# Optimization experiments

Hardware: AMD Instinct MI355X
Metric: run time of the kernel (lower is better)

## Reference

```python
import jax, jax.numpy as jnp
import numpy as np

M, K, N, E = 8192, 1024, 1024, 8  # total tokens, in-dim, out-dim, experts/segments


def setup_inputs() -> dict:
    key = jax.random.key(0)
    k1, k2, k3 = jax.random.split(key, 3)
    a = jax.random.normal(k1, (M, K), dtype=jnp.float32)
    b = jax.random.normal(k2, (E, N, K), dtype=jnp.float32) * 0.02  # column-major per-expert weights
    c = jnp.zeros((M, N), dtype=jnp.float32)
    inner = jnp.sort(jax.random.randint(k3, (E - 1,), 0, M, dtype=jnp.int32))
    seg_indptr = jnp.concatenate([
        jnp.zeros((1,), jnp.int32), inner, jnp.full((1,), M, jnp.int32)
    ])  # [E+1], monotone, covers [0, M)
    weight_indices = jnp.arange(E, dtype=jnp.int32)
    return {
        "a": a, "b": b, "c": c,
        "batch_size": E, "weight_column_major": 1,
        "seg_indptr": seg_indptr, "weight_indices": weight_indices,
    }


def reference(a, b, c, batch_size, weight_column_major, seg_indptr, weight_indices):
    # Grouped GEMM: for each contiguous segment s of rows [seg_indptr[s], seg_indptr[s+1]),
    # c[rows] = a[rows] @ b[weight_indices[s]].T  (b is [E, N, K], column-major weights).
    assert weight_column_major
    rows = jnp.arange(a.shape[0])[:, None]  # [M, 1]
    out = c
    for s in range(batch_size):  # fixed small loop over experts/segments
        b_e = jnp.take(b, weight_indices[s], axis=0)  # [N, K]
        seg_out = a @ b_e.T                            # [M, N]
        mask = (rows >= seg_indptr[s]) & (rows < seg_indptr[s + 1])
        out = jnp.where(mask, seg_out, out)
    return out
```

## Files before the change

kernel.cpp:

```cpp
#include <hip/hip_runtime.h>
#include <hip/hip_bf16.h>
#include <stdint.h>

#define MDIM 8192
#define KDIM 1024
#define NDIM 1024
#define NEXP 8
#define BM 256
#define BN 256
#define BK 64
#define LDSS 40

typedef __attribute__((ext_vector_type(8))) short bf16x8;
typedef __attribute__((ext_vector_type(4))) float floatx4;
typedef __attribute__((ext_vector_type(8))) unsigned short ushort8;

static __device__ __forceinline__ unsigned short f2b(float f) {
    unsigned int u = __float_as_uint(f);
    return (unsigned short)((u + 0x7fffu + ((u >> 16) & 1u)) >> 16);
}

__global__ __launch_bounds__(256)
void cvt_bf16(const float* __restrict__ a, const float* __restrict__ b,
              unsigned short* __restrict__ wa, unsigned short* __restrict__ wb)
{
    const long t  = (long)blockIdx.x * 256 + threadIdx.x;
    const long NA = (long)MDIM * KDIM / 8;
    const float* src; unsigned short* dst; long v;
    if (t < NA) { src = a; dst = wa; v = t; }
    else        { src = b; dst = wb; v = t - NA; }
    const float4 lo = ((const float4*)src)[2 * v];
    const float4 hi = ((const float4*)src)[2 * v + 1];
    ushort8 o;
    o[0] = f2b(lo.x); o[1] = f2b(lo.y); o[2] = f2b(lo.z); o[3] = f2b(lo.w);
    o[4] = f2b(hi.x); o[5] = f2b(hi.y); o[6] = f2b(hi.z); o[7] = f2b(hi.w);
    ((ushort8*)dst)[v] = o;
}

#define GLDS(gp, lp) __builtin_amdgcn_global_load_lds(                        \
    (const __attribute__((address_space(1))) unsigned int*)(gp),              \
    (__attribute__((address_space(3))) unsigned int*)(lp), 16, 0, 0)

#define BAR asm volatile("s_barrier" ::: "memory")


__global__ __launch_bounds__(512, 2)
void grouped_gemm_v8(const unsigned short* __restrict__ A,
                     const unsigned short* __restrict__ B,
                     const int* __restrict__ seg_indptr,
                     const int* __restrict__ widx,
                     float* __restrict__ c)
{
    alignas(16) __shared__ unsigned short As0[BM * BK], As1[BM * BK];
    alignas(16) __shared__ unsigned short Bs0[BN * BK], Bs1[BN * BK];

    const int orig = (int)blockIdx.x;
    const int xcd = orig & 7, lin = orig >> 3;
    const int bid = (xcd < 4 ? xcd * 20 : 80 + (xcd - 4) * 19) + lin;

    const int NTN = NDIM / BN;
    int rem = bid;
    int s = -1, m0 = 0, seg_end = 0, n0 = 0;
    for (int i = 0; i < NEXP; ++i) {
        int ps = seg_indptr[i], pe = seg_indptr[i + 1];
        int nt = ((pe - ps + BM - 1) / BM) * NTN;
        if (rem < nt) { s = i; m0 = ps + (rem / NTN) * BM; n0 = (rem % NTN) * BN; seg_end = pe; break; }
        rem -= nt;
    }
    if (s < 0) return;

    const unsigned short* __restrict__ be = B + (size_t)widx[s] * (size_t)(NDIM * KDIM);

    const int tid  = (int)threadIdx.x;
    const int wave = tid >> 6;
    const int lane = tid & 63;

    const int srow = tid >> 3;
    const int gch  = ((tid & 7) ^ (srow & 7)) * 8;
    const unsigned short* ap[4];
    const unsigned short* bp[4];
#pragma unroll
    for (int j = 0; j < 4; ++j) {
        int ra = m0 + j * 64 + srow; if (ra >= MDIM) ra = MDIM - 1;
        ap[j] = A  + (size_t)ra * KDIM + gch;
        bp[j] = be + (size_t)(n0 + j * 64 + srow) * KDIM + gch;
    }
    const int ldso = wave * 512;

    const int wm = (wave >> 2) * 128;
    const int wn = (wave & 3) * 64;
    const int fr   = lane & 15;
    const int quad = lane >> 4;
    const int fro0 = ((0 * 4 + quad) ^ (fr & 7)) * 8;
    const int fro1 = ((1 * 4 + quad) ^ (fr & 7)) * 8;

    floatx4 acc[8][4] = {};
    bf16x8 b0[4], b1[4];

#define STAGE_A(DST, h, koff) do {                                            \
        GLDS(ap[2 * (h) + 0] + (koff), &DST[(2 * (h) + 0) * 4096 + ldso]);    \
        GLDS(ap[2 * (h) + 1] + (koff), &DST[(2 * (h) + 1) * 4096 + ldso]);    \
    } while (0)
#define STAGE_B(DST, h, koff) do {                                            \
        GLDS(bp[2 * (h) + 0] + (koff), &DST[(2 * (h) + 0) * 4096 + ldso]);    \
        GLDS(bp[2 * (h) + 1] + (koff), &DST[(2 * (h) + 1) * 4096 + ldso]);    \
    } while (0)

#define PHASE(AS, BS, Q, RB, STG, WV)                                         \
    do {                                                                      \
        bf16x8 af0  = *reinterpret_cast<const bf16x8*>(                       \
            &AS[(wm + (2 * (Q) + 0) * 16 + fr) * BK + fro0]);                 \
        bf16x8 af1  = *reinterpret_cast<const bf16x8*>(                       \
            &AS[(wm + (2 * (Q) + 1) * 16 + fr) * BK + fro0]);                 \
        bf16x8 af0b = *reinterpret_cast<const bf16x8*>(                       \
            &AS[(wm + (2 * (Q) + 0) * 16 + fr) * BK + fro1]);                 \
        bf16x8 af1b = *reinterpret_cast<const bf16x8*>(                       \
            &AS[(wm + (2 * (Q) + 1) * 16 + fr) * BK + fro1]);                 \
        if (RB) {                                                             \
            _Pragma("unroll")                                                 \
            for (int ni = 0; ni < 4; ++ni) {                                  \
                b0[ni] = *reinterpret_cast<const bf16x8*>(                    \
                    &BS[(wn + ni * 16 + fr) * BK + fro0]);                    \
                b1[ni] = *reinterpret_cast<const bf16x8*>(                    \
                    &BS[(wn + ni * 16 + fr) * BK + fro1]);                    \
            }                                                                 \
        }                                                                     \
        STG;                                                                  \
        if (RB) asm volatile("s_waitcnt lgkmcnt(8)" ::: "memory");            \
        BAR;                                                                  \
        asm volatile("s_waitcnt lgkmcnt(0)" ::: "memory");                    \
        __builtin_amdgcn_s_setprio(1);                                        \
        _Pragma("unroll")                                                     \
        for (int ni = 0; ni < 4; ++ni) {                                      \
            acc[2 * (Q) + 0][ni] = __builtin_amdgcn_mfma_f32_16x16x32_bf16(   \
                af0,  b0[ni], acc[2 * (Q) + 0][ni], 0, 0, 0);                 \
            acc[2 * (Q) + 1][ni] = __builtin_amdgcn_mfma_f32_16x16x32_bf16(   \
                af1,  b0[ni], acc[2 * (Q) + 1][ni], 0, 0, 0);                 \
            acc[2 * (Q) + 0][ni] = __builtin_amdgcn_mfma_f32_16x16x32_bf16(   \
                af0b, b1[ni], acc[2 * (Q) + 0][ni], 0, 0, 0);                 \
            acc[2 * (Q) + 1][ni] = __builtin_amdgcn_mfma_f32_16x16x32_bf16(   \
                af1b, b1[ni], acc[2 * (Q) + 1][ni], 0, 0, 0);                 \
        }                                                                     \
        __builtin_amdgcn_s_setprio(0);                                        \
        WV;                                                                   \
        BAR;                                                                  \
    } while (0)

#define VM4 asm volatile("s_waitcnt vmcnt(4)" ::: "memory")

    STAGE_A(As0, 0, 0); STAGE_A(As0, 1, 0);
    STAGE_B(Bs0, 0, 0); STAGE_B(Bs0, 1, 0);
    STAGE_B(Bs1, 0, BK); STAGE_B(Bs1, 1, BK);
    asm volatile("s_waitcnt vmcnt(4)" ::: "memory");
    BAR;

#pragma unroll 1
    for (int ii = 0; ii < 8; ++ii) {
        const int t   = 2 * ii;
        const int kA1 = (t + 1) * BK;
        const int kN2 = ((t + 2) & 15) * BK;
        const int kN3 = ((t + 3) & 15) * BK;
        PHASE(As0, Bs0, 0, true,  STAGE_A(As1, 0, kA1), (void)0);
        PHASE(As0, Bs0, 1, false, STAGE_A(As1, 1, kA1), (void)0);
        PHASE(As0, Bs0, 2, false, STAGE_B(Bs0, 0, kN2), (void)0);
        PHASE(As0, Bs0, 3, false, STAGE_B(Bs0, 1, kN2), VM4);
        PHASE(As1, Bs1, 0, true,  STAGE_A(As0, 0, kN2), (void)0);
        PHASE(As1, Bs1, 1, false, STAGE_A(As0, 1, kN2), (void)0);
        PHASE(As1, Bs1, 2, false, STAGE_B(Bs1, 0, kN3), (void)0);
        PHASE(As1, Bs1, 3, false, STAGE_B(Bs1, 1, kN3), VM4);
    }
    asm volatile("s_waitcnt vmcnt(0)" ::: "memory");

#pragma unroll
    for (int mi = 0; mi < 8; ++mi) {
        const int rbase = m0 + wm + mi * 16 + quad * 4;
#pragma unroll
        for (int ni = 0; ni < 4; ++ni) {
            const int col = n0 + wn + ni * 16 + fr;
#pragma unroll
            for (int j = 0; j < 4; ++j) {
                const int row = rbase + j;
                if (row < seg_end)
                    c[(size_t)row * NDIM + col] = acc[mi][ni][j];
            }
        }
    }
#undef STAGE_A
#undef STAGE_B
#undef PHASE
#undef VM4
}

__global__ __launch_bounds__(256, 2)
void grouped_gemm_fused(const float* __restrict__ a, const float* __restrict__ b,
                        const int* __restrict__ seg_indptr, const int* __restrict__ widx,
                        float* __restrict__ c)
{
    __shared__ unsigned short Asf[128 * LDSS];
    __shared__ unsigned short Bsf[128 * LDSS];
    const int NT = NDIM / 128;
    int rem = (int)blockIdx.x;
    int s = -1, m0 = 0, seg_end = 0, n0 = 0;
    for (int i = 0; i < NEXP; ++i) {
        int ps = seg_indptr[i], pe = seg_indptr[i + 1];
        int nt = ((pe - ps + 127) / 128) * NT;
        if (rem < nt) { s = i; m0 = ps + (rem / NT) * 128; n0 = (rem % NT) * 128; seg_end = pe; break; }
        rem -= nt;
    }
    if (s < 0) return;
    const float* __restrict__ be = b + (size_t)widx[s] * (size_t)(NDIM * KDIM);
    const int tid = (int)threadIdx.x;
    const int r0 = tid >> 3;
    const int kc = (tid & 7) * 4;
    int arow[4];
#pragma unroll
    for (int u = 0; u < 4; ++u) {
        int r = m0 + r0 + 32 * u;
        arow[u] = r < MDIM ? r : MDIM - 1;
    }
    const int lane = tid & 63;
    const int wave = tid >> 6;
    const int wm = (wave & 1) * 64;
    const int wn = (wave >> 1) * 64;
    const int fr = lane & 15;
    const int quad = lane >> 4;
    floatx4 acc[4][4] = {};
    float4 av[4], bv[4];
#pragma unroll
    for (int u = 0; u < 4; ++u) {
        av[u] = *reinterpret_cast<const float4*>(a + (size_t)arow[u] * KDIM + kc);
        bv[u] = *reinterpret_cast<const float4*>(be + (size_t)(n0 + r0 + 32 * u) * KDIM + kc);
    }
    for (int k0 = 0; k0 < KDIM; k0 += 32) {
        __syncthreads();
#pragma unroll
        for (int u = 0; u < 4; ++u) {
            ushort4 ua, ub;
            ua.x = f2b(av[u].x); ua.y = f2b(av[u].y); ua.z = f2b(av[u].z); ua.w = f2b(av[u].w);
            ub.x = f2b(bv[u].x); ub.y = f2b(bv[u].y); ub.z = f2b(bv[u].z); ub.w = f2b(bv[u].w);
            *reinterpret_cast<ushort4*>(&Asf[(r0 + 32 * u) * LDSS + kc]) = ua;
            *reinterpret_cast<ushort4*>(&Bsf[(r0 + 32 * u) * LDSS + kc]) = ub;
        }
        const int kn = (k0 + 32 < KDIM) ? (k0 + 32) : 0;
#pragma unroll
        for (int u = 0; u < 4; ++u) {
            av[u] = *reinterpret_cast<const float4*>(a + (size_t)arow[u] * KDIM + kn + kc);
            bv[u] = *reinterpret_cast<const float4*>(be + (size_t)(n0 + r0 + 32 * u) * KDIM + kn + kc);
        }
        __syncthreads();
        bf16x8 af[4], bf[4];
#pragma unroll
        for (int mi = 0; mi < 4; ++mi)
            af[mi] = *reinterpret_cast<const bf16x8*>(&Asf[(wm + mi * 16 + fr) * LDSS + quad * 8]);
#pragma unroll
        for (int ni = 0; ni < 4; ++ni)
            bf[ni] = *reinterpret_cast<const bf16x8*>(&Bsf[(wn + ni * 16 + fr) * LDSS + quad * 8]);
#pragma unroll
        for (int mi = 0; mi < 4; ++mi)
#pragma unroll
            for (int ni = 0; ni < 4; ++ni)
                acc[mi][ni] = __builtin_amdgcn_mfma_f32_16x16x32_bf16(af[mi], bf[ni], acc[mi][ni], 0, 0, 0);
    }
#pragma unroll
    for (int mi = 0; mi < 4; ++mi) {
        const int rbase = m0 + wm + mi * 16 + quad * 4;
#pragma unroll
        for (int ni = 0; ni < 4; ++ni) {
            const int col = n0 + wn + ni * 16 + fr;
#pragma unroll
            for (int j = 0; j < 4; ++j) {
                const int row = rbase + j;
                if (row < seg_end)
                    c[(size_t)row * NDIM + col] = acc[mi][ni][j];
            }
        }
    }
}

extern "C" void kernel_launch(void* const* d_in, const int* in_sizes, int n_in,
                              void* d_out, int out_size, void* d_ws, size_t ws_size,
                              hipStream_t stream) {
    const float* a          = (const float*)d_in[0];
    const float* b          = (const float*)d_in[1];
    const int*   seg_indptr = (const int*)d_in[5];
    const int*   widx       = (const int*)d_in[6];
    float*       out        = (float*)d_out;

    const size_t need = (size_t)(MDIM + NEXP * NDIM) * KDIM * sizeof(unsigned short);
    if (ws_size >= need) {
        unsigned short* wa = (unsigned short*)d_ws;
        unsigned short* wb = wa + (size_t)MDIM * KDIM;
        hipLaunchKernelGGL(cvt_bf16, dim3(8192), dim3(256), 0, stream, a, b, wa, wb);
        hipLaunchKernelGGL(grouped_gemm_v8, dim3(156), dim3(512), 0, stream,
                           wa, wb, seg_indptr, widx, out);
    } else {
        hipLaunchKernelGGL(grouped_gemm_fused, dim3(568), dim3(256), 0, stream,
                           a, b, seg_indptr, widx, out);
    }
}
```

Before: 167.4 us.

## Replace phased interleaved staging with simple double-buffered stage/compute loop

Replaces the eight-phase schedule with a plain double-buffered loop. In the old schedule, A and B tile loads were split across phases with priority hints and fine-grained lgkmcnt waits. Now each half-iteration issues the full next-tile load, waits with vmcnt(8), barriers, and then runs the whole 64-wide K-step of MFMAs. This simplifies the code and cuts the number of barriers per tile. The risk is weaker overlap between loads and math: the vmcnt(8) right after issue appears to wait only for the current buffer's loads, and the setprio hints are gone.

```diff
diff --git a/kernel.cpp b/kernel.cpp
--- a/kernel.cpp
+++ b/kernel.cpp
@@ -45,7 +45,7 @@
 
 
 __global__ __launch_bounds__(512, 2)
-void grouped_gemm_v8(const unsigned short* __restrict__ A,
+void grouped_gemm_v9(const unsigned short* __restrict__ A,
                      const unsigned short* __restrict__ B,
                      const int* __restrict__ seg_indptr,
                      const int* __restrict__ widx,
@@ -95,79 +95,66 @@
     const int fro1 = ((1 * 4 + quad) ^ (fr & 7)) * 8;
 
     floatx4 acc[8][4] = {};
-    bf16x8 b0[4], b1[4];
-
-#define STAGE_A(DST, h, koff) do {                                            \
-        GLDS(ap[2 * (h) + 0] + (koff), &DST[(2 * (h) + 0) * 4096 + ldso]);    \
-        GLDS(ap[2 * (h) + 1] + (koff), &DST[(2 * (h) + 1) * 4096 + ldso]);    \
+
+#define STAGE(AD, BD, koff) do {                                              \
+        _Pragma("unroll")                                                     \
+        for (int j = 0; j < 4; ++j) {                                         \
+            GLDS(ap[j] + (koff), &AD[j * 4096 + ldso]);                       \
+            GLDS(bp[j] + (koff), &BD[j * 4096 + ldso]);                       \
+        }                                                                     \
     } while (0)
-#define STAGE_B(DST, h, koff) do {                                            \
-        GLDS(bp[2 * (h) + 0] + (koff), &DST[(2 * (h) + 0) * 4096 + ldso]);    \
-        GLDS(bp[2 * (h) + 1] + (koff), &DST[(2 * (h) + 1) * 4096 + ldso]);    \
-    } while (0)
-
-#define PHASE(AS, BS, Q, RB, STG, WV)                                         \
+
+#define COMPUTE(AS, BS)                                                       \
     do {                                                                      \
-        bf16x8 af0  = *reinterpret_cast<const bf16x8*>(                       \
-            &AS[(wm + (2 * (Q) + 0) * 16 + fr) * BK + fro0]);                 \
-        bf16x8 af1  = *reinterpret_cast<const bf16x8*>(                       \
-            &AS[(wm + (2 * (Q) + 1) * 16 + fr) * BK + fro0]);                 \
-        bf16x8 af0b = *reinterpret_cast<const bf16x8*>(                       \
-            &AS[(wm + (2 * (Q) + 0) * 16 + fr) * BK + fro1]);                 \
-        bf16x8 af1b = *reinterpret_cast<const bf16x8*>(                       \
-            &AS[(wm + (2 * (Q) + 1) * 16 + fr) * BK + fro1]);                 \
-        if (RB) {                                                             \
+        bf16x8 b0[4], b1[4];                                                  \
+        _Pragma("unroll")                                                     \
+        for (int ni = 0; ni < 4; ++ni) {                                      \
+            b0[ni] = *reinterpret_cast<const bf16x8*>(                        \
+                &BS[(wn + ni * 16 + fr) * BK + fro0]);                        \
+            b1[ni] = *reinterpret_cast<const bf16x8*>(                        \
+                &BS[(wn + ni * 16 + fr) * BK + fro1]);                        \
+        }                                                                     \
+        _Pragma("unroll")                                                     \
+        for (int q = 0; q < 4; ++q) {                                         \
+            bf16x8 af0  = *reinterpret_cast<const bf16x8*>(                   \
+                &AS[(wm + (2 * q + 0) * 16 + fr) * BK + fro0]);               \
+            bf16x8 af1  = *reinterpret_cast<const bf16x8*>(                   \
+                &AS[(wm + (2 * q + 1) * 16 + fr) * BK + fro0]);               \
+            bf16x8 af0b = *reinterpret_cast<const bf16x8*>(                   \
+                &AS[(wm + (2 * q + 0) * 16 + fr) * BK + fro1]);               \
+            bf16x8 af1b = *reinterpret_cast<const bf16x8*>(                   \
+                &AS[(wm + (2 * q + 1) * 16 + fr) * BK + fro1]);               \
             _Pragma("unroll")                                                 \
             for (int ni = 0; ni < 4; ++ni) {                                  \
-                b0[ni] = *reinterpret_cast<const bf16x8*>(                    \
-                    &BS[(wn + ni * 16 + fr) * BK + fro0]);                    \
-                b1[ni] = *reinterpret_cast<const bf16x8*>(                    \
-                    &BS[(wn + ni * 16 + fr) * BK + fro1]);                    \
+                acc[2 * q + 0][ni] = __builtin_amdgcn_mfma_f32_16x16x32_bf16( \
+                    af0,  b0[ni], acc[2 * q + 0][ni], 0, 0, 0);               \
+                acc[2 * q + 1][ni] = __builtin_amdgcn_mfma_f32_16x16x32_bf16( \
+                    af1,  b0[ni], acc[2 * q + 1][ni], 0, 0, 0);               \
+                acc[2 * q + 0][ni] = __builtin_amdgcn_mfma_f32_16x16x32_bf16( \
+                    af0b, b1[ni], acc[2 * q + 0][ni], 0, 0, 0);               \
+                acc[2 * q + 1][ni] = __builtin_amdgcn_mfma_f32_16x16x32_bf16( \
+                    af1b, b1[ni], acc[2 * q + 1][ni], 0, 0, 0);               \
             }                                                                 \
         }                                                                     \
-        STG;                                                                  \
-        if (RB) asm volatile("s_waitcnt lgkmcnt(8)" ::: "memory");            \
-        BAR;                                                                  \
-        asm volatile("s_waitcnt lgkmcnt(0)" ::: "memory");                    \
-        __builtin_amdgcn_s_setprio(1);                                        \
-        _Pragma("unroll")                                                     \
-        for (int ni = 0; ni < 4; ++ni) {                                      \
-            acc[2 * (Q) + 0][ni] = __builtin_amdgcn_mfma_f32_16x16x32_bf16(   \
-                af0,  b0[ni], acc[2 * (Q) + 0][ni], 0, 0, 0);                 \
-            acc[2 * (Q) + 1][ni] = __builtin_amdgcn_mfma_f32_16x16x32_bf16(   \
-                af1,  b0[ni], acc[2 * (Q) + 1][ni], 0, 0, 0);                 \
-            acc[2 * (Q) + 0][ni] = __builtin_amdgcn_mfma_f32_16x16x32_bf16(   \
-                af0b, b1[ni], acc[2 * (Q) + 0][ni], 0, 0, 0);                 \
-            acc[2 * (Q) + 1][ni] = __builtin_amdgcn_mfma_f32_16x16x32_bf16(   \
-                af1b, b1[ni], acc[2 * (Q) + 1][ni], 0, 0, 0);                 \
-        }                                                                     \
-        __builtin_amdgcn_s_setprio(0);                                        \
-        WV;                                                                   \
-        BAR;                                                                  \
     } while (0)
 
-#define VM4 asm volatile("s_waitcnt vmcnt(4)" ::: "memory")
-
-    STAGE_A(As0, 0, 0); STAGE_A(As0, 1, 0);
-    STAGE_B(Bs0, 0, 0); STAGE_B(Bs0, 1, 0);
-    STAGE_B(Bs1, 0, BK); STAGE_B(Bs1, 1, BK);
-    asm volatile("s_waitcnt vmcnt(4)" ::: "memory");
-    BAR;
+#define VM8 asm volatile("s_waitcnt vmcnt(8)" ::: "memory")
+
+    STAGE(As0, Bs0, 0);
 
 #pragma unroll 1
     for (int ii = 0; ii < 8; ++ii) {
-        const int t   = 2 * ii;
-        const int kA1 = (t + 1) * BK;
-        const int kN2 = ((t + 2) & 15) * BK;
-        const int kN3 = ((t + 3) & 15) * BK;
-        PHASE(As0, Bs0, 0, true,  STAGE_A(As1, 0, kA1), (void)0);
-        PHASE(As0, Bs0, 1, false, STAGE_A(As1, 1, kA1), (void)0);
-        PHASE(As0, Bs0, 2, false, STAGE_B(Bs0, 0, kN2), (void)0);
-        PHASE(As0, Bs0, 3, false, STAGE_B(Bs0, 1, kN2), VM4);
-        PHASE(As1, Bs1, 0, true,  STAGE_A(As0, 0, kN2), (void)0);
-        PHASE(As1, Bs1, 1, false, STAGE_A(As0, 1, kN2), (void)0);
-        PHASE(As1, Bs1, 2, false, STAGE_B(Bs1, 0, kN3), (void)0);
-        PHASE(As1, Bs1, 3, false, STAGE_B(Bs1, 1, kN3), VM4);
+        const int t = 2 * ii;
+        BAR;
+        STAGE(As1, Bs1, (t + 1) * BK);
+        VM8;
+        BAR;
+        COMPUTE(As0, Bs0);
+        BAR;
+        STAGE(As0, Bs0, ((t + 2) & 15) * BK);
+        VM8;
+        BAR;
+        COMPUTE(As1, Bs1);
     }
     asm volatile("s_waitcnt vmcnt(0)" ::: "memory");
 
@@ -185,10 +172,9 @@
             }
         }
     }
-#undef STAGE_A
-#undef STAGE_B
-#undef PHASE
-#undef VM4
+#undef STAGE
+#undef COMPUTE
+#undef VM8
 }
 
 __global__ __launch_bounds__(256, 2)
@@ -291,7 +277,7 @@
         unsigned short* wa = (unsigned short*)d_ws;
         unsigned short* wb = wa + (size_t)MDIM * KDIM;
         hipLaunchKernelGGL(cvt_bf16, dim3(8192), dim3(256), 0, stream, a, b, wa, wb);
-        hipLaunchKernelGGL(grouped_gemm_v8, dim3(156), dim3(512), 0, stream,
+        hipLaunchKernelGGL(grouped_gemm_v9, dim3(156), dim3(512), 0, stream,
                            wa, wb, seg_indptr, widx, out);
     } else {
         hipLaunchKernelGGL(grouped_gemm_fused, dim3(568), dim3(256), 0, stream,
```

Result: no change. 164.7 us (-1.6%).
